# Kernel tuning notes

Hardware: AMD Instinct MI355X
Metric: run time of the kernel (lower is better)

The kernel has to match this reference:

```python
import jax, jax.numpy as jnp
import numpy as np
from math import comb

# --- module hyperparameters (from init_kwargs / module-level constants) ---
F = 32          # features
NITER = 3       # num_iterations
NB = 16         # num_basis_functions
NDCM = 4        # n_dcm
CUTOFF = 4.0
MAXZ = 17       # max_atomic_number
NC = 9          # (max_degree+1)^2 spherical components, max_degree=2
DEG = np.array([0, 1, 1, 1, 2, 2, 2, 2, 2])  # degree l of each component
BINOM = jnp.asarray([comb(NB - 1, k) for k in range(NB)], dtype=jnp.float32)


def _np_sph9(x, y, z):
    # real spherical harmonics up to l=2 on the unit sphere (numpy, for Gaunt table)
    c0 = 0.28209479177387814; c1 = 0.4886025119029199
    c2a = 1.0925484305920792; c2b = 0.31539156525252005; c2c = 0.5462742152960396
    return np.stack([c0 * np.ones_like(x), c1 * y, c1 * z, c1 * x,
                     c2a * x * y, c2a * y * z, c2b * (3.0 * z * z - 1.0),
                     c2a * x * z, c2c * (x * x - y * y)], axis=0)


def _gaunt():
    # real Gaunt (Clebsch-Gordan-type) coefficients G[a,b,c] = int Y_a Y_b Y_c dOmega
    # via Gauss-Legendre (cos theta) x midpoint (phi) quadrature -- exact for l<=2 products
    ct, wt = np.polynomial.legendre.leggauss(64)
    nph = 256
    phi = (np.arange(nph) + 0.5) * (2.0 * np.pi / nph)
    st = np.sqrt(1.0 - ct ** 2)
    x = st[:, None] * np.cos(phi)[None, :]
    y = st[:, None] * np.sin(phi)[None, :]
    z = np.broadcast_to(ct[:, None], x.shape)
    w = (wt[:, None] * (2.0 * np.pi / nph)) * np.ones((1, nph))
    Y = _np_sph9(x, y, z)
    G = np.einsum('aij,bij,cij,ij->abc', Y, Y, Y, w)
    G[np.abs(G) < 1e-6] = 0.0
    return G

CG = jnp.asarray(_gaunt(), dtype=jnp.float32)  # (9, 9, 9), sparse


def _sph9(u):
    # u: (E, 3) unit vectors -> (E, 9)
    x, y, z = u[:, 0], u[:, 1], u[:, 2]
    c0 = 0.28209479177387814; c1 = 0.4886025119029199
    c2a = 1.0925484305920792; c2b = 0.31539156525252005; c2c = 0.5462742152960396
    return jnp.stack([jnp.full_like(x, c0), c1 * y, c1 * z, c1 * x,
                      c2a * x * y, c2a * y * z, c2b * (3.0 * z * z - 1.0),
                      c2a * x * z, c2c * (x * x - y * y)], axis=-1)


def _radial(r):
    # reciprocal Bernstein radial basis * smooth cutoff; r: (E,) -> (E, NB)
    u = 1.0 / (1.0 + r)
    k = jnp.arange(NB, dtype=jnp.float32)
    rb = BINOM * u[:, None] ** k * (1.0 - u[:, None]) ** (NB - 1 - k)
    t = r / CUTOFF
    den = jnp.where(t < 1.0, 1.0 - t * t, 1.0)
    fc = jnp.where(t < 1.0, jnp.exp(-t * t / den), 0.0)  # smooth_cutoff
    return rb * fc[:, None]


def _equiv_dense(x, W, b=None):
    # per-degree linear (equivariant Dense): x (N, 9, Fin), W (3, Fin, Fout); bias on l=0 only
    y = jnp.einsum('ncf,cfg->ncg', x, W[DEG])
    if b is not None:
        y = y.at[:, 0, :].add(b)
    return y


def _tp(xs, bf):
    # Gaunt tensor-product contraction: out[e,c,f] = sum_ab CG[a,b,c] xs[e,a,f] bf[e,b,f]
    # loop over the 9 fixed output components to avoid an (E,9,9,F) intermediate
    out = []
    for c in range(NC):
        t = jnp.einsum('eaf,ab->ebf', xs, CG[:, :, c])
        out.append(jnp.sum(t * bf, axis=1))
    return jnp.stack(out, axis=1)


def _forward(atomic_numbers, positions, dst_idx, src_idx, embed, Wb, W1, b1, W2, b2,
             Wt00, Wt11, Wmono, element_bias):
    n = atomic_numbers.shape[0]
    disp = positions[src_idx] - positions[dst_idx]                 # (E, 3) gather
    r = jnp.sqrt(jnp.sum(disp * disp, axis=-1) + 1e-12)            # safe norm
    u = disp / r[:, None]
    basis = _sph9(u)[:, :, None] * _radial(r)[:, None, :]          # (E, 9, NB)
    x = jnp.zeros((n, NC, F), dtype=positions.dtype).at[:, 0, :].set(embed[atomic_numbers])
    for i in range(NITER):  # message passing iterations
        bf = jnp.einsum('ebn,bng->ebg', basis, Wb[i][DEG])         # per-degree radial->feature mix (E,9,F)
        msg = _tp(x[src_idx], bf)                                  # gather src + tensor product
        y = x + jax.ops.segment_sum(msg, dst_idx, num_segments=n)  # scatter-aggregate + residual add
        y = _equiv_dense(y, W1[i], b1[i])
        y = jax.nn.silu(y)
        y = _equiv_dense(y, W2[i], b2[i])
        x = x + y                                                  # residual update
    # TensorDense to n_dcm channels, then readout heads
    mono = (x[:, 0, :] @ Wt00) @ Wmono + element_bias[atomic_numbers][:, None]  # (N, NDCM)
    dip = jnp.einsum('ncf,fg->ncg', x[:, 1:4, :], Wt11)            # (N, 3, NDCM) vector channel
    dip = jnp.clip(jax.nn.silu(dip), -0.3, 0.3) + positions[:, :, None]
    return mono, dip


def setup_inputs():
    key = jax.random.key(0)
    ks = jax.random.split(key, 12)
    N, E = 10000, 160000
    return {
        'atomic_numbers': jax.random.randint(ks[0], (N,), 0, MAXZ + 1),
        'positions': jax.random.normal(ks[1], (N, 3), jnp.float32) * 3.0,
        'dst_idx': jax.random.randint(ks[2], (E,), 0, N),
        'src_idx': jax.random.randint(ks[3], (E,), 0, N),
        'embed': jax.random.normal(ks[4], (MAXZ + 1, F), jnp.float32),
        'Wb': jax.random.normal(ks[5], (NITER, 3, NB, F), jnp.float32) / np.sqrt(NB).astype(np.float32),
        'W1': jax.random.normal(ks[6], (NITER, 3, F, F), jnp.float32) / np.sqrt(F).astype(np.float32),
        'b1': jnp.zeros((NITER, F), jnp.float32),
        'W2': jax.random.normal(ks[7], (NITER, 3, F, F), jnp.float32) / np.sqrt(F).astype(np.float32),
        'b2': jnp.zeros((NITER, F), jnp.float32),
        'Wt00': jax.random.normal(ks[8], (F, NDCM), jnp.float32) / np.sqrt(F).astype(np.float32),
        'Wt11': jax.random.normal(ks[9], (F, NDCM), jnp.float32) / np.sqrt(F).astype(np.float32),
        'Wmono': jax.random.normal(ks[10], (NDCM, NDCM), jnp.float32) / np.sqrt(NDCM).astype(np.float32),
        'element_bias': jnp.zeros((MAXZ + 1,), jnp.float32),
    }


def reference(atomic_numbers, positions, dst_idx, src_idx, embed, Wb, W1, b1, W2, b2,
              Wt00, Wt11, Wmono, element_bias):
    return _forward(atomic_numbers, positions, dst_idx, src_idx, embed, Wb, W1, b1, W2, b2,
                    Wt00, Wt11, Wmono, element_bias)
```

## Files before the change

kernel.cpp:

```cpp
#include <hip/hip_runtime.h>
#include <hip/hip_bf16.h>


#define NITER 3
#define BCAP  64

#define OFF_WB    0
#define OFF_W1    4608
#define OFF_B1    13824
#define OFF_W2    13920
#define OFF_B2    23136
#define OFF_WT00  23232
#define OFF_WT11  23360
#define OFF_WMONO 23488
#define OFF_EB    23504
#define OFF_EMB   23522
#define WC_TOTAL  24098

__device__ __forceinline__ float b2f(const __hip_bfloat16 v) { return __bfloat162float(v); }

#define KC0 0.28209479177387814f
#define KG1 0.21850968611841584f
#define KG2 0.12615662610100802f
#define KG3 0.18022375157287861f
#define KG4 0.09011187578643931f
#define KG5 0.15607834722743988f

__device__ __forceinline__ float ldany(const void* p, int i, bool f32) {
    return f32 ? ((const float*)p)[i] : b2f(((const __hip_bfloat16*)p)[i]);
}

__device__ __forceinline__ bool wave_sniff(const void* pos) {
    const __hip_bfloat16* p = (const __hip_bfloat16*)pos;
    int lane = threadIdx.x & 63;
    int bad = 0;
    #pragma unroll
    for (int k = 0; k < 4; k++) {
        float v = b2f(p[lane + k*64]);
        bad |= !(fabsf(v) < 1.0e6f);
    }
    return __ballot(bad) != 0ull;
}

__global__ void setup_kernel(const void* pos, const void* Wb, const void* W1,
        const void* b1, const void* W2, const void* b2, const void* Wt00,
        const void* Wt11, const void* Wmono, const void* eb, const void* emb,
        const int* __restrict__ an,
        float* __restrict__ posf, float* __restrict__ wc,
        float* __restrict__ x, int N) {
    bool f32 = wave_sniff(pos);
    int i = blockIdx.x * blockDim.x + threadIdx.x;
    int np = N * 3;
    if (i < np) { posf[i] = ldany(pos, i, f32); return; }
    int j = i - np;
    if (j < WC_TOTAL) {
        const void* src; int rel;
        if      (j < OFF_W1)    { src = Wb;    rel = j; }
        else if (j < OFF_B1)    { src = W1;    rel = j - OFF_W1; }
        else if (j < OFF_W2)    { src = b1;    rel = j - OFF_B1; }
        else if (j < OFF_B2)    { src = W2;    rel = j - OFF_W2; }
        else if (j < OFF_WT00)  { src = b2;    rel = j - OFF_B2; }
        else if (j < OFF_WT11)  { src = Wt00;  rel = j - OFF_WT00; }
        else if (j < OFF_WMONO) { src = Wt11;  rel = j - OFF_WT11; }
        else if (j < OFF_EB)    { src = Wmono; rel = j - OFF_WMONO; }
        else if (j < OFF_EMB)   { src = eb;    rel = j - OFF_EB; }
        else                    { src = emb;   rel = j - OFF_EMB; }
        wc[j] = ldany(src, rel, f32);
        return;
    }
    j -= WC_TOTAL;
    if (j < N * 32) {
        int n = j >> 5, rem = j & 31;
        x[(size_t)n * 288 + rem] = ldany(emb, an[n] * 32 + rem, f32);
    }
}

__device__ __forceinline__ bool edge_geom(float dx, float dy, float dz,
                                          float* sp, float* rad) {
    float r2 = dx*dx + dy*dy + dz*dz + 1e-12f;
    if (r2 >= 16.0f) return false;
    float r  = sqrtf(r2);
    float t2 = r2 * 0.0625f;
    float fc = __expf(-t2 / (1.0f - t2));
    float u = 1.0f / (1.0f + r);
    float v = 1.0f - u;
    const float BIN[16] = {1.f,15.f,105.f,455.f,1365.f,3003.f,5005.f,6435.f,
                           6435.f,5005.f,3003.f,1365.f,455.f,105.f,15.f,1.f};
    float vp[16];
    vp[0] = 1.0f;
    #pragma unroll
    for (int k = 1; k < 16; k++) vp[k] = vp[k-1] * v;
    float up = 1.0f;
    #pragma unroll
    for (int n = 0; n < 16; n++) { rad[n] = BIN[n] * up * vp[15-n] * fc; up *= u; }
    float ir = 1.0f / r;
    float ux = dx*ir, uy = dy*ir, uz = dz*ir;
    const float c0 = 0.28209479177387814f, c1 = 0.4886025119029199f;
    const float c2a = 1.0925484305920792f, c2b = 0.31539156525252005f, c2c = 0.5462742152960396f;
    sp[0] = c0;
    sp[1] = c1*uy; sp[2] = c1*uz; sp[3] = c1*ux;
    sp[4] = c2a*ux*uy; sp[5] = c2a*uy*uz; sp[6] = c2b*(3.0f*uz*uz - 1.0f);
    sp[7] = c2a*ux*uz; sp[8] = c2c*(ux*ux - uy*uy);
    return true;
}

__global__ void fill_csr_kernel(const float* __restrict__ posf,
        const int* __restrict__ srcI, const int* __restrict__ dstI,
        float* __restrict__ geo2, int* __restrict__ cur, int E) {
    int e = blockIdx.x * blockDim.x + threadIdx.x;
    if (e >= E) return;
    int s = srcI[e], d = dstI[e];
    float sp[9], rad[16];
    if (!edge_geom(posf[s*3+0] - posf[d*3+0],
                   posf[s*3+1] - posf[d*3+1],
                   posf[s*3+2] - posf[d*3+2], sp, rad)) return;
    int slot = atomicAdd(&cur[d], 1);
    float* gp = geo2 + ((size_t)d * BCAP + slot) * 32;
    gp[0] = __int_as_float(s);
    gp[1] = 0.0f;
    #pragma unroll
    for (int a = 0; a < 9; a++) gp[2 + a] = sp[a];
    gp[11] = 0.0f;
    #pragma unroll
    for (int k = 0; k < 16; k++) gp[16 + k] = rad[k];
}

template <bool FIRST, bool LAST>
__global__ __launch_bounds__(256) void edge_gather_kernel(
        const float* __restrict__ x, float* __restrict__ y,
        const float* __restrict__ geo2, const int* __restrict__ cur,
        const float* __restrict__ Wbi, int N) {
    int f = threadIdx.x & 31;
    int n = (blockIdx.x * blockDim.x + threadIdx.x) >> 5;
    if (n >= N) return;
    float w0[16], w1[16], w2[16];
    #pragma unroll
    for (int k = 0; k < 16; k++) {
        w0[k] = Wbi[(0*16 + k)*32 + f];
        w1[k] = Wbi[(1*16 + k)*32 + f];
        w2[k] = Wbi[(2*16 + k)*32 + f];
    }
    float A0=0.f,A1=0.f,A2=0.f,A3=0.f,A4=0.f,A5=0.f,A6=0.f,A7=0.f,A8=0.f;
    int beg = n * BCAP, end = beg + cur[n];
    for (int e = beg; e < end; e++) {
        const float4* gp = (const float4*)(geo2 + (size_t)e * 32);
        float4 h0 = gp[0], h1 = gp[1], h2 = gp[2];
        float4 r0 = gp[4], r1 = gp[5], r2 = gp[6], r3 = gp[7];
        int s = __float_as_int(h0.x);
        float rad[16] = {r0.x,r0.y,r0.z,r0.w, r1.x,r1.y,r1.z,r1.w,
                         r2.x,r2.y,r2.z,r2.w, r3.x,r3.y,r3.z,r3.w};
        float rw0 = 0.f, rw1 = 0.f, rw2 = 0.f;
        #pragma unroll
        for (int k = 0; k < 16; k++) {
            rw0 = fmaf(rad[k], w0[k], rw0);
            rw1 = fmaf(rad[k], w1[k], rw1);
            rw2 = fmaf(rad[k], w2[k], rw2);
        }
        float B0 = h0.z*rw0;
        float B1 = h0.w*rw1, B2 = h1.x*rw1, B3 = h1.y*rw1;
        float B4 = h1.z*rw2, B5 = h1.w*rw2, B6 = h2.x*rw2,
              B7 = h2.y*rw2, B8 = h2.z*rw2;
        const float* xp = x + (size_t)s*288 + f;
        if (FIRST) {
            float X0 = xp[0];
            float k0 = KC0 * X0;
            A0 += k0*B0; A1 += k0*B1; A2 += k0*B2; A3 += k0*B3; A4 += k0*B4;
            A5 += k0*B5; A6 += k0*B6; A7 += k0*B7; A8 += k0*B8;
        } else {
            float X0 = xp[0],   X1 = xp[32],  X2 = xp[64],  X3 = xp[96],  X4 = xp[128];
            float X5 = xp[160], X6 = xp[192], X7 = xp[224], X8 = xp[256];
            A0 += KC0*(X0*B0 + X1*B1 + X2*B2 + X3*B3 + X4*B4 + X5*B5 + X6*B6 + X7*B7 + X8*B8);
            A1 += KC0*(X0*B1 + X1*B0) + KG1*(X3*B4 + X4*B3 + X2*B5 + X5*B2)
                - KG2*(X1*B6 + X6*B1) - KG1*(X1*B8 + X8*B1);
            A2 += KC0*(X0*B2 + X2*B0) + KG1*(X1*B5 + X5*B1 + X3*B7 + X7*B3)
                + 2.0f*KG2*(X2*B6 + X6*B2);
            A3 += KC0*(X0*B3 + X3*B0) + KG1*(X1*B4 + X4*B1 + X2*B7 + X7*B2)
                - KG2*(X3*B6 + X6*B3) + KG1*(X3*B8 + X8*B3);
            if (!LAST) {
                A4 += KC0*(X0*B4 + X4*B0) + KG1*(X1*B3 + X3*B1) + KG5*(X5*B7 + X7*B5)
                    - KG3*(X4*B6 + X6*B4);
                A5 += KC0*(X0*B5 + X5*B0) + KG1*(X1*B2 + X2*B1) + KG5*(X4*B7 + X7*B4)
                    + KG4*(X5*B6 + X6*B5) - KG5*(X5*B8 + X8*B5);
                A6 += KC0*(X0*B6 + X6*B0) - KG2*X1*B1 + 2.0f*KG2*X2*B2 - KG2*X3*B3
                    - KG3*X4*B4 + KG4*X5*B5 + KG3*X6*B6 + KG4*X7*B7 - KG3*X8*B8;
                A7 += KC0*(X0*B7 + X7*B0) + KG1*(X2*B3 + X3*B2) + KG5*(X4*B5 + X5*B4)
                    + KG4*(X6*B7 + X7*B6) + KG5*(X7*B8 + X8*B7);
                A8 += KC0*(X0*B8 + X8*B0) - KG1*X1*B1 + KG1*X3*B3 - KG5*X5*B5 + KG5*X7*B7
                    - KG3*(X6*B8 + X8*B6);
            }
        }
    }
    float* yp = y + (size_t)n * 288 + f;
    yp[0]   = A0; yp[32]  = A1; yp[64]  = A2; yp[96]  = A3;
    if (!LAST) {
        yp[128] = A4; yp[160] = A5; yp[192] = A6; yp[224] = A7; yp[256] = A8;
    }
}

template <bool FIRST>
__global__ __launch_bounds__(256) void atom_kernel(
        float* __restrict__ x, const float* __restrict__ y,
        const float* __restrict__ W1i, const float* __restrict__ b1i,
        const float* __restrict__ W2i, const float* __restrict__ b2i,
        int N) {
    __shared__ float sm[4][64*33];
    int lane  = threadIdx.x & 63;
    int wslot = threadIdx.x >> 6;
    int u = __builtin_amdgcn_readfirstlane(blockIdx.x * 4 + wslot);
    int t = u / 9;
    int c = u - t * 9;
    int d = (c == 0) ? 0 : ((c < 4) ? 1 : 2);
    const float* W1 = W1i + d * 1024;
    const float* W2 = W2i + d * 1024;
    float* tile = sm[wslot];
    bool usex = (!FIRST) || (c == 0);
    float4 xr4[8];
    #pragma unroll
    for (int k = 0; k < 8; k++) {
        int e  = lane * 4 + k * 256;
        int al = e >> 5, f = e & 31;
        int ag = t * 64 + al;
        float4 s = make_float4(0.f, 0.f, 0.f, 0.f);
        float4 xv = make_float4(0.f, 0.f, 0.f, 0.f);
        if (ag < N) {
            if (usex) xv = *(const float4*)(x + (size_t)ag * 288 + c * 32 + f);
            float4 yv = *(const float4*)(y + (size_t)ag * 288 + c * 32 + f);
            s = make_float4(xv.x + yv.x, xv.y + yv.y, xv.z + yv.z, xv.w + yv.w);
        }
        xr4[k] = xv;
        *(float4*)(tile + al * 33 + f) = s;
    }
    __syncthreads();
    float yin[32];
    #pragma unroll
    for (int k = 0; k < 8; k++) {
        float4 v = *(const float4*)(tile + lane * 33 + 4 * k);
        yin[4*k+0] = v.x; yin[4*k+1] = v.y; yin[4*k+2] = v.z; yin[4*k+3] = v.w;
    }
    float acc[32];
    #pragma unroll
    for (int g = 0; g < 32; g++) acc[g] = (c == 0) ? b1i[g] : 0.0f;
    #pragma unroll 4
    for (int fi = 0; fi < 32; fi++) {
        float v = yin[fi];
        #pragma unroll
        for (int g = 0; g < 32; g++) acc[g] = fmaf(v, W1[fi*32 + g], acc[g]);
    }
    #pragma unroll
    for (int g = 0; g < 32; g++)
        acc[g] = acc[g] * __builtin_amdgcn_rcpf(1.0f + __expf(-acc[g]));
    float out[32];
    #pragma unroll
    for (int g = 0; g < 32; g++) out[g] = (c == 0) ? b2i[g] : 0.0f;
    #pragma unroll 4
    for (int fi = 0; fi < 32; fi++) {
        float v = acc[fi];
        #pragma unroll
        for (int g = 0; g < 32; g++) out[g] = fmaf(v, W2[fi*32 + g], out[g]);
    }
    __syncthreads();
    #pragma unroll
    for (int k = 0; k < 8; k++)
        *(float4*)(tile + lane * 33 + 4 * k) =
            make_float4(out[4*k+0], out[4*k+1], out[4*k+2], out[4*k+3]);
    __syncthreads();
    #pragma unroll
    for (int k = 0; k < 8; k++) {
        int e  = lane * 4 + k * 256;
        int al = e >> 5, f = e & 31;
        int ag = t * 64 + al;
        if (ag < N) {
            float4 dv = *(const float4*)(tile + al * 33 + f);
            float4 xv = xr4[k];
            *(float4*)(x + (size_t)ag * 288 + c * 32 + f) =
                make_float4(xv.x + dv.x, xv.y + dv.y, xv.z + dv.z, xv.w + dv.w);
        }
    }
}

__global__ __launch_bounds__(256) void atom_readout_kernel(
        const float* __restrict__ x, const float* __restrict__ y,
        const float* __restrict__ W1i, const float* __restrict__ b1i,
        const float* __restrict__ W2i, const float* __restrict__ b2i,
        const int* __restrict__ an, const float* __restrict__ posf,
        const float* __restrict__ wc, const void* __restrict__ pos,
        void* __restrict__ out_, int N) {
    bool f32 = wave_sniff(pos);
    __shared__ float sm[4][64*33];
    int lane  = threadIdx.x & 63;
    int wslot = threadIdx.x >> 6;
    int c = __builtin_amdgcn_readfirstlane(wslot);
    int t = blockIdx.x;
    int d = (c == 0) ? 0 : 1;
    const float* W1 = W1i + d * 1024;
    const float* W2 = W2i + d * 1024;
    float* tile = sm[wslot];
    float4 xr4[8];
    #pragma unroll
    for (int k = 0; k < 8; k++) {
        int e  = lane * 4 + k * 256;
        int al = e >> 5, f = e & 31;
        int ag = t * 64 + al;
        float4 s = make_float4(0.f, 0.f, 0.f, 0.f);
        float4 xv = make_float4(0.f, 0.f, 0.f, 0.f);
        if (ag < N) {
            xv = *(const float4*)(x + (size_t)ag * 288 + c * 32 + f);
            float4 yv = *(const float4*)(y + (size_t)ag * 288 + c * 32 + f);
            s = make_float4(xv.x + yv.x, xv.y + yv.y, xv.z + yv.z, xv.w + yv.w);
        }
        xr4[k] = xv;
        *(float4*)(tile + al * 33 + f) = s;
    }
    __syncthreads();
    float yin[32];
    #pragma unroll
    for (int k = 0; k < 8; k++) {
        float4 v = *(const float4*)(tile + lane * 33 + 4 * k);
        yin[4*k+0] = v.x; yin[4*k+1] = v.y; yin[4*k+2] = v.z; yin[4*k+3] = v.w;
    }
    float acc[32];
    #pragma unroll
    for (int g = 0; g < 32; g++) acc[g] = (c == 0) ? b1i[g] : 0.0f;
    #pragma unroll 4
    for (int fi = 0; fi < 32; fi++) {
        float v = yin[fi];
        #pragma unroll
        for (int g = 0; g < 32; g++) acc[g] = fmaf(v, W1[fi*32 + g], acc[g]);
    }
    #pragma unroll
    for (int g = 0; g < 32; g++)
        acc[g] = acc[g] * __builtin_amdgcn_rcpf(1.0f + __expf(-acc[g]));
    float out[32];
    #pragma unroll
    for (int g = 0; g < 32; g++) out[g] = (c == 0) ? b2i[g] : 0.0f;
    #pragma unroll 4
    for (int fi = 0; fi < 32; fi++) {
        float v = acc[fi];
        #pragma unroll
        for (int g = 0; g < 32; g++) out[g] = fmaf(v, W2[fi*32 + g], out[g]);
    }
    __syncthreads();
    #pragma unroll
    for (int k = 0; k < 8; k++)
        *(float4*)(tile + lane * 33 + 4 * k) =
            make_float4(out[4*k+0], out[4*k+1], out[4*k+2], out[4*k+3]);
    __syncthreads();
    #pragma unroll
    for (int k = 0; k < 8; k++) {
        int e  = lane * 4 + k * 256;
        int al = e >> 5, f = e & 31;
        float4 dv = *(const float4*)(tile + al * 33 + f);
        float4 xv = xr4[k];
        *(float4*)(tile + al * 33 + f) =
            make_float4(xv.x + dv.x, xv.y + dv.y, xv.z + dv.z, xv.w + dv.w);
    }
    __syncthreads();
    if (threadIdx.x < 64) {
        int a  = threadIdx.x;
        int ag = t * 64 + a;
        if (ag < N) {
            const float* Wt00  = wc + OFF_WT00;
            const float* Wt11  = wc + OFF_WT11;
            const float* Wmono = wc + OFF_WMONO;
            const float* x0 = sm[0] + a * 33;
            float q[4] = {0.f, 0.f, 0.f, 0.f};
            for (int f = 0; f < 32; f++) {
                float xv = x0[f];
                #pragma unroll
                for (int j = 0; j < 4; j++) q[j] = fmaf(xv, Wt00[f*4 + j], q[j]);
            }
            float ebv = wc[OFF_EB + an[ag]];
            #pragma unroll
            for (int m = 0; m < 4; m++) {
                float accm = ebv;
                #pragma unroll
                for (int j = 0; j < 4; j++) accm = fmaf(q[j], Wmono[j*4 + m], accm);
                if (f32) ((float*)out_)[ag*4 + m] = accm;
                else ((__hip_bfloat16*)out_)[ag*4 + m] = __float2bfloat16(accm);
            }
            #pragma unroll
            for (int cc = 0; cc < 3; cc++) {
                float pc = posf[ag*3 + cc];
                const float* xc = sm[1 + cc] + a * 33;
                float dq[4] = {0.f, 0.f, 0.f, 0.f};
                for (int f = 0; f < 32; f++) {
                    float xv = xc[f];
                    #pragma unroll
                    for (int m = 0; m < 4; m++) dq[m] = fmaf(xv, Wt11[f*4 + m], dq[m]);
                }
                #pragma unroll
                for (int m = 0; m < 4; m++) {
                    float v = dq[m];
                    v = v * __builtin_amdgcn_rcpf(1.0f + __expf(-v));
                    v = fminf(fmaxf(v, -0.3f), 0.3f);
                    v += pc;
                    if (f32) ((float*)out_)[N*4 + ag*12 + cc*4 + m] = v;
                    else ((__hip_bfloat16*)out_)[N*4 + ag*12 + cc*4 + m] = __float2bfloat16(v);
                }
            }
        }
    }
}

__global__ void zero_kernel(float4* __restrict__ b, int n) {
    int i = blockIdx.x * blockDim.x + threadIdx.x;
    int stride = gridDim.x * blockDim.x;
    float4 z = make_float4(0.f, 0.f, 0.f, 0.f);
    for (; i < n; i += stride) b[i] = z;
}

__global__ __launch_bounds__(256) void edge_inline_kernel(
        const float* __restrict__ x, float* __restrict__ y,
        const float* __restrict__ posf,
        const int* __restrict__ srcI, const int* __restrict__ dstI,
        const float* __restrict__ Wbi, int E) {
    int f  = threadIdx.x & 31;
    int hw = (blockIdx.x * blockDim.x + threadIdx.x) >> 5;
    int nhw = gridDim.x * (blockDim.x >> 5);
    float w0[16], w1[16], w2[16];
    #pragma unroll
    for (int n = 0; n < 16; n++) {
        w0[n] = Wbi[(0*16 + n)*32 + f];
        w1[n] = Wbi[(1*16 + n)*32 + f];
        w2[n] = Wbi[(2*16 + n)*32 + f];
    }
    for (int e = hw; e < E; e += nhw) {
        int s = srcI[e], d = dstI[e];
        float sp[9], rad[16];
        if (!edge_geom(posf[s*3+0] - posf[d*3+0],
                       posf[s*3+1] - posf[d*3+1],
                       posf[s*3+2] - posf[d*3+2], sp, rad)) continue;
        float rw0 = 0.f, rw1 = 0.f, rw2 = 0.f;
        #pragma unroll
        for (int n = 0; n < 16; n++) {
            rw0 = fmaf(rad[n], w0[n], rw0);
            rw1 = fmaf(rad[n], w1[n], rw1);
            rw2 = fmaf(rad[n], w2[n], rw2);
        }
        float B0 = sp[0]*rw0;
        float B1 = sp[1]*rw1, B2 = sp[2]*rw1, B3 = sp[3]*rw1;
        float B4 = sp[4]*rw2, B5 = sp[5]*rw2, B6 = sp[6]*rw2,
              B7 = sp[7]*rw2, B8 = sp[8]*rw2;
        const float* xp = x + (size_t)s*288 + f;
        float X0 = xp[0],   X1 = xp[32],  X2 = xp[64],  X3 = xp[96],  X4 = xp[128];
        float X5 = xp[160], X6 = xp[192], X7 = xp[224], X8 = xp[256];
        float* yp = y + (size_t)d*288 + f;
        float m;
        m = KC0*(X0*B0 + X1*B1 + X2*B2 + X3*B3 + X4*B4 + X5*B5 + X6*B6 + X7*B7 + X8*B8);
        unsafeAtomicAdd(yp + 0, m);
        m = KC0*(X0*B1 + X1*B0) + KG1*(X3*B4 + X4*B3 + X2*B5 + X5*B2)
          - KG2*(X1*B6 + X6*B1) - KG1*(X1*B8 + X8*B1);
        unsafeAtomicAdd(yp + 32, m);
        m = KC0*(X0*B2 + X2*B0) + KG1*(X1*B5 + X5*B1 + X3*B7 + X7*B3)
          + 2.0f*KG2*(X2*B6 + X6*B2);
        unsafeAtomicAdd(yp + 64, m);
        m = KC0*(X0*B3 + X3*B0) + KG1*(X1*B4 + X4*B1 + X2*B7 + X7*B2)
          - KG2*(X3*B6 + X6*B3) + KG1*(X3*B8 + X8*B3);
        unsafeAtomicAdd(yp + 96, m);
        m = KC0*(X0*B4 + X4*B0) + KG1*(X1*B3 + X3*B1) + KG5*(X5*B7 + X7*B5)
          - KG3*(X4*B6 + X6*B4);
        unsafeAtomicAdd(yp + 128, m);
        m = KC0*(X0*B5 + X5*B0) + KG1*(X1*B2 + X2*B1) + KG5*(X4*B7 + X7*B4)
          + KG4*(X5*B6 + X6*B5) - KG5*(X5*B8 + X8*B5);
        unsafeAtomicAdd(yp + 160, m);
        m = KC0*(X0*B6 + X6*B0) - KG2*X1*B1 + 2.0f*KG2*X2*B2 - KG2*X3*B3
          - KG3*X4*B4 + KG4*X5*B5 + KG3*X6*B6 + KG4*X7*B7 - KG3*X8*B8;
        unsafeAtomicAdd(yp + 192, m);
        m = KC0*(X0*B7 + X7*B0) + KG1*(X2*B3 + X3*B2) + KG5*(X4*B5 + X5*B4)
          + KG4*(X6*B7 + X7*B6) + KG5*(X7*B8 + X8*B7);
        unsafeAtomicAdd(yp + 224, m);
        m = KC0*(X0*B8 + X8*B0) - KG1*X1*B1 + KG1*X3*B3 - KG5*X5*B5 + KG5*X7*B7
          - KG3*(X6*B8 + X8*B6);
        unsafeAtomicAdd(yp + 256, m);
    }
}

__global__ void readout_kernel(const float* __restrict__ x,
        const int* __restrict__ an, const float* __restrict__ posf,
        const float* __restrict__ wc, const void* __restrict__ pos,
        void* __restrict__ out, int N) {
    bool f32 = wave_sniff(pos);
    int n = blockIdx.x * blockDim.x + threadIdx.x;
    if (n >= N) return;
    const float* Wt00  = wc + OFF_WT00;
    const float* Wt11  = wc + OFF_WT11;
    const float* Wmono = wc + OFF_WMONO;
    const float* xb = x + (size_t)n * 288;
    float q[4] = {0.f, 0.f, 0.f, 0.f};
    for (int f = 0; f < 32; f++) {
        float xv = xb[f];
        #pragma unroll
        for (int j = 0; j < 4; j++) q[j] = fmaf(xv, Wt00[f*4 + j], q[j]);
    }
    float ebv = wc[OFF_EB + an[n]];
    #pragma unroll
    for (int m = 0; m < 4; m++) {
        float acc = ebv;
        #pragma unroll
        for (int j = 0; j < 4; j++) acc = fmaf(q[j], Wmono[j*4 + m], acc);
        if (f32) ((float*)out)[n*4 + m] = acc;
        else ((__hip_bfloat16*)out)[n*4 + m] = __float2bfloat16(acc);
    }
    #pragma unroll
    for (int c = 0; c < 3; c++) {
        float pc = posf[n*3 + c];
        const float* xc = xb + (1 + c)*32;
        float dq[4] = {0.f, 0.f, 0.f, 0.f};
        for (int f = 0; f < 32; f++) {
            float xv = xc[f];
            #pragma unroll
            for (int m = 0; m < 4; m++) dq[m] = fmaf(xv, Wt11[f*4 + m], dq[m]);
        }
        #pragma unroll
        for (int m = 0; m < 4; m++) {
            float v = dq[m];
            v = v * __builtin_amdgcn_rcpf(1.0f + __expf(-v));
            v = fminf(fmaxf(v, -0.3f), 0.3f);
            v += pc;
            if (f32) ((float*)out)[N*4 + n*12 + c*4 + m] = v;
            else ((__hip_bfloat16*)out)[N*4 + n*12 + c*4 + m] = __float2bfloat16(v);
        }
    }
}

extern "C" void kernel_launch(void* const* d_in, const int* in_sizes, int n_in,
                              void* d_out, int out_size, void* d_ws, size_t ws_size,
                              hipStream_t stream) {
    const int* an    = (const int*)d_in[0];
    const void* pos  = d_in[1];
    const int* dstI  = (const int*)d_in[2];
    const int* srcI  = (const int*)d_in[3];
    const void* embed= d_in[4];
    const void* Wb   = d_in[5];
    const void* W1   = d_in[6];
    const void* b1   = d_in[7];
    const void* W2   = d_in[8];
    const void* b2   = d_in[9];
    const void* Wt00 = d_in[10];
    const void* Wt11 = d_in[11];
    const void* Wmono= d_in[12];
    const void* eb   = d_in[13];
    int N = in_sizes[0];
    int E = in_sizes[2];

    float* x    = (float*)d_ws;
    float* y    = x + (size_t)N * 288;
    float* posf = y + (size_t)N * 288;
    float* wc   = posf + (size_t)N * 3;
    int* cur    = (int*)(wc + WC_TOTAL);
    uintptr_t ga = ((uintptr_t)(cur + N) + 127) & ~(uintptr_t)127;
    float* geo2 = (float*)ga;
    size_t need = (uintptr_t)(geo2 + (size_t)N * BCAP * 32) - (uintptr_t)d_ws;
    bool use_csr = (ws_size >= need);

    hipMemsetAsync(cur, 0, sizeof(int) * (size_t)N, stream);
    if (!use_csr)
        zero_kernel<<<512, 256, 0, stream>>>((float4*)x, N * 72);
    {
        int tot = N * 3 + WC_TOTAL + N * 32;
        setup_kernel<<<(tot + 255)/256, 256, 0, stream>>>(
            pos, Wb, W1, b1, W2, b2, Wt00, Wt11, Wmono, eb, embed,
            an, posf, wc, x, N);
    }
    int ntiles = (N + 63) / 64;
    if (use_csr) {
        fill_csr_kernel<<<(E + 255)/256, 256, 0, stream>>>(posf, srcI, dstI,
                                                           geo2, cur, E);
        int gblocks = (N + 7) / 8;
        for (int i = 0; i < NITER; i++) {
            const float* Wbi = wc + OFF_WB + (size_t)i*1536;
            const float* W1i = wc + OFF_W1 + (size_t)i*3072;
            const float* b1i = wc + OFF_B1 + (size_t)i*32;
            const float* W2i = wc + OFF_W2 + (size_t)i*3072;
            const float* b2i = wc + OFF_B2 + (size_t)i*32;
            if (i == 0) {
                edge_gather_kernel<true,false><<<gblocks, 256, 0, stream>>>(
                    x, y, geo2, cur, Wbi, N);
                atom_kernel<true><<<(ntiles*9 + 3)/4, 256, 0, stream>>>(
                    x, y, W1i, b1i, W2i, b2i, N);
            } else if (i == NITER - 1) {
                edge_gather_kernel<false,true><<<gblocks, 256, 0, stream>>>(
                    x, y, geo2, cur, Wbi, N);
                atom_readout_kernel<<<ntiles, 256, 0, stream>>>(
                    x, y, W1i, b1i, W2i, b2i, an, posf, wc, pos, d_out, N);
            } else {
                edge_gather_kernel<false,false><<<gblocks, 256, 0, stream>>>(
                    x, y, geo2, cur, Wbi, N);
                atom_kernel<false><<<(ntiles*9 + 3)/4, 256, 0, stream>>>(
                    x, y, W1i, b1i, W2i, b2i, N);
            }
        }
    } else {
        int ablocks = (ntiles * 9 + 3) / 4;
        for (int i = 0; i < NITER; i++) {
            zero_kernel<<<512, 256, 0, stream>>>((float4*)y, N * 72);
            edge_inline_kernel<<<2048, 256, 0, stream>>>(x, y, posf, srcI, dstI,
                wc + OFF_WB + (size_t)i*1536, E);
            atom_kernel<false><<<ablocks, 256, 0, stream>>>(x, y,
                wc + OFF_W1 + (size_t)i*3072, wc + OFF_B1 + (size_t)i*32,
                wc + OFF_W2 + (size_t)i*3072, wc + OFF_B2 + (size_t)i*32, N);
        }
        readout_kernel<<<(N + 255)/256, 256, 0, stream>>>(x, an, posf, wc, pos,
                                                          d_out, N);
    }
}
```

Before: 223.4 us.

## Fuse edge gather and atom MLP per iteration; fold CSR fill into setup

Each message-passing iteration now runs as one kernel per 32-atom tile: it gathers edge messages into shared memory and then applies the per-degree MLP update. Node features ping-pong between two buffers, which removes the intermediate y round-trip through global memory. Edge geometry and CSR bucket filling move into the setup kernel, dropping a separate launch. Both kernel launches and global traffic go down, but the fused kernel uses a larger shared-memory slab and has less parallelism per block.

```diff
diff --git a/kernel.cpp b/kernel.cpp
--- a/kernel.cpp
+++ b/kernel.cpp
@@ -42,12 +42,43 @@
     return __ballot(bad) != 0ull;
 }
 
+__device__ __forceinline__ bool edge_geom(float dx, float dy, float dz,
+                                          float* sp, float* rad) {
+    float r2 = dx*dx + dy*dy + dz*dz + 1e-12f;
+    if (r2 >= 16.0f) return false;
+    float r  = sqrtf(r2);
+    float t2 = r2 * 0.0625f;
+    float fc = __expf(-t2 / (1.0f - t2));
+    float u = 1.0f / (1.0f + r);
+    float v = 1.0f - u;
+    const float BIN[16] = {1.f,15.f,105.f,455.f,1365.f,3003.f,5005.f,6435.f,
+                           6435.f,5005.f,3003.f,1365.f,455.f,105.f,15.f,1.f};
+    float vp[16];
+    vp[0] = 1.0f;
+    #pragma unroll
+    for (int k = 1; k < 16; k++) vp[k] = vp[k-1] * v;
+    float up = 1.0f;
+    #pragma unroll
+    for (int n = 0; n < 16; n++) { rad[n] = BIN[n] * up * vp[15-n] * fc; up *= u; }
+    float ir = 1.0f / r;
+    float ux = dx*ir, uy = dy*ir, uz = dz*ir;
+    const float c0 = 0.28209479177387814f, c1 = 0.4886025119029199f;
+    const float c2a = 1.0925484305920792f, c2b = 0.31539156525252005f, c2c = 0.5462742152960396f;
+    sp[0] = c0;
+    sp[1] = c1*uy; sp[2] = c1*uz; sp[3] = c1*ux;
+    sp[4] = c2a*ux*uy; sp[5] = c2a*uy*uz; sp[6] = c2b*(3.0f*uz*uz - 1.0f);
+    sp[7] = c2a*ux*uz; sp[8] = c2c*(ux*ux - uy*uy);
+    return true;
+}
+
 __global__ void setup_kernel(const void* pos, const void* Wb, const void* W1,
         const void* b1, const void* W2, const void* b2, const void* Wt00,
         const void* Wt11, const void* Wmono, const void* eb, const void* emb,
         const int* __restrict__ an,
+        const int* __restrict__ srcI, const int* __restrict__ dstI,
         float* __restrict__ posf, float* __restrict__ wc,
-        float* __restrict__ x, int N) {
+        float* __restrict__ x, float* __restrict__ geo2, int* __restrict__ cur,
+        int N, int E, int use_csr) {
     bool f32 = wave_sniff(pos);
     int i = blockIdx.x * blockDim.x + threadIdx.x;
     int np = N * 3;
@@ -72,330 +103,246 @@
     if (j < N * 32) {
         int n = j >> 5, rem = j & 31;
         x[(size_t)n * 288 + rem] = ldany(emb, an[n] * 32 + rem, f32);
-    }
-}
-
-__device__ __forceinline__ bool edge_geom(float dx, float dy, float dz,
-                                          float* sp, float* rad) {
-    float r2 = dx*dx + dy*dy + dz*dz + 1e-12f;
-    if (r2 >= 16.0f) return false;
-    float r  = sqrtf(r2);
-    float t2 = r2 * 0.0625f;
-    float fc = __expf(-t2 / (1.0f - t2));
-    float u = 1.0f / (1.0f + r);
-    float v = 1.0f - u;
-    const float BIN[16] = {1.f,15.f,105.f,455.f,1365.f,3003.f,5005.f,6435.f,
-                           6435.f,5005.f,3003.f,1365.f,455.f,105.f,15.f,1.f};
-    float vp[16];
-    vp[0] = 1.0f;
-    #pragma unroll
-    for (int k = 1; k < 16; k++) vp[k] = vp[k-1] * v;
-    float up = 1.0f;
-    #pragma unroll
-    for (int n = 0; n < 16; n++) { rad[n] = BIN[n] * up * vp[15-n] * fc; up *= u; }
-    float ir = 1.0f / r;
-    float ux = dx*ir, uy = dy*ir, uz = dz*ir;
-    const float c0 = 0.28209479177387814f, c1 = 0.4886025119029199f;
-    const float c2a = 1.0925484305920792f, c2b = 0.31539156525252005f, c2c = 0.5462742152960396f;
-    sp[0] = c0;
-    sp[1] = c1*uy; sp[2] = c1*uz; sp[3] = c1*ux;
-    sp[4] = c2a*ux*uy; sp[5] = c2a*uy*uz; sp[6] = c2b*(3.0f*uz*uz - 1.0f);
-    sp[7] = c2a*ux*uz; sp[8] = c2c*(ux*ux - uy*uy);
-    return true;
-}
-
-__global__ void fill_csr_kernel(const float* __restrict__ posf,
-        const int* __restrict__ srcI, const int* __restrict__ dstI,
-        float* __restrict__ geo2, int* __restrict__ cur, int E) {
-    int e = blockIdx.x * blockDim.x + threadIdx.x;
-    if (e >= E) return;
-    int s = srcI[e], d = dstI[e];
-    float sp[9], rad[16];
-    if (!edge_geom(posf[s*3+0] - posf[d*3+0],
-                   posf[s*3+1] - posf[d*3+1],
-                   posf[s*3+2] - posf[d*3+2], sp, rad)) return;
-    int slot = atomicAdd(&cur[d], 1);
-    float* gp = geo2 + ((size_t)d * BCAP + slot) * 32;
-    gp[0] = __int_as_float(s);
-    gp[1] = 0.0f;
-    #pragma unroll
-    for (int a = 0; a < 9; a++) gp[2 + a] = sp[a];
-    gp[11] = 0.0f;
-    #pragma unroll
-    for (int k = 0; k < 16; k++) gp[16 + k] = rad[k];
+        return;
+    }
+    j -= N * 32;
+    if (j < E && use_csr) {
+        int s = srcI[j], d = dstI[j];
+        float sp[9], rad[16];
+        if (!edge_geom(ldany(pos, s*3+0, f32) - ldany(pos, d*3+0, f32),
+                       ldany(pos, s*3+1, f32) - ldany(pos, d*3+1, f32),
+                       ldany(pos, s*3+2, f32) - ldany(pos, d*3+2, f32),
+                       sp, rad)) return;
+        int slot = atomicAdd(&cur[d], 1);
+        float* gp = geo2 + ((size_t)d * BCAP + slot) * 32;
+        gp[0] = __int_as_float(s);
+        gp[1] = 0.0f;
+        #pragma unroll
+        for (int a = 0; a < 9; a++) gp[2 + a] = sp[a];
+        gp[11] = 0.0f;
+        #pragma unroll
+        for (int k = 0; k < 16; k++) gp[16 + k] = rad[k];
+    }
 }
 
 template <bool FIRST, bool LAST>
-__global__ __launch_bounds__(256) void edge_gather_kernel(
-        const float* __restrict__ x, float* __restrict__ y,
+__global__ __launch_bounds__(256) void fused_iter_kernel(
+        const float* __restrict__ xin, float* __restrict__ xout,
         const float* __restrict__ geo2, const int* __restrict__ cur,
-        const float* __restrict__ Wbi, int N) {
-    int f = threadIdx.x & 31;
-    int n = (blockIdx.x * blockDim.x + threadIdx.x) >> 5;
-    if (n >= N) return;
-    float w0[16], w1[16], w2[16];
-    #pragma unroll
-    for (int k = 0; k < 16; k++) {
-        w0[k] = Wbi[(0*16 + k)*32 + f];
-        w1[k] = Wbi[(1*16 + k)*32 + f];
-        w2[k] = Wbi[(2*16 + k)*32 + f];
-    }
-    float A0=0.f,A1=0.f,A2=0.f,A3=0.f,A4=0.f,A5=0.f,A6=0.f,A7=0.f,A8=0.f;
-    int beg = n * BCAP, end = beg + cur[n];
-    for (int e = beg; e < end; e++) {
-        const float4* gp = (const float4*)(geo2 + (size_t)e * 32);
-        float4 h0 = gp[0], h1 = gp[1], h2 = gp[2];
-        float4 r0 = gp[4], r1 = gp[5], r2 = gp[6], r3 = gp[7];
-        int s = __float_as_int(h0.x);
-        float rad[16] = {r0.x,r0.y,r0.z,r0.w, r1.x,r1.y,r1.z,r1.w,
-                         r2.x,r2.y,r2.z,r2.w, r3.x,r3.y,r3.z,r3.w};
-        float rw0 = 0.f, rw1 = 0.f, rw2 = 0.f;
-        #pragma unroll
-        for (int k = 0; k < 16; k++) {
-            rw0 = fmaf(rad[k], w0[k], rw0);
-            rw1 = fmaf(rad[k], w1[k], rw1);
-            rw2 = fmaf(rad[k], w2[k], rw2);
-        }
-        float B0 = h0.z*rw0;
-        float B1 = h0.w*rw1, B2 = h1.x*rw1, B3 = h1.y*rw1;
-        float B4 = h1.z*rw2, B5 = h1.w*rw2, B6 = h2.x*rw2,
-              B7 = h2.y*rw2, B8 = h2.z*rw2;
-        const float* xp = x + (size_t)s*288 + f;
-        if (FIRST) {
-            float X0 = xp[0];
-            float k0 = KC0 * X0;
-            A0 += k0*B0; A1 += k0*B1; A2 += k0*B2; A3 += k0*B3; A4 += k0*B4;
-            A5 += k0*B5; A6 += k0*B6; A7 += k0*B7; A8 += k0*B8;
-        } else {
-            float X0 = xp[0],   X1 = xp[32],  X2 = xp[64],  X3 = xp[96],  X4 = xp[128];
-            float X5 = xp[160], X6 = xp[192], X7 = xp[224], X8 = xp[256];
-            A0 += KC0*(X0*B0 + X1*B1 + X2*B2 + X3*B3 + X4*B4 + X5*B5 + X6*B6 + X7*B7 + X8*B8);
-            A1 += KC0*(X0*B1 + X1*B0) + KG1*(X3*B4 + X4*B3 + X2*B5 + X5*B2)
-                - KG2*(X1*B6 + X6*B1) - KG1*(X1*B8 + X8*B1);
-            A2 += KC0*(X0*B2 + X2*B0) + KG1*(X1*B5 + X5*B1 + X3*B7 + X7*B3)
-                + 2.0f*KG2*(X2*B6 + X6*B2);
-            A3 += KC0*(X0*B3 + X3*B0) + KG1*(X1*B4 + X4*B1 + X2*B7 + X7*B2)
-                - KG2*(X3*B6 + X6*B3) + KG1*(X3*B8 + X8*B3);
-            if (!LAST) {
-                A4 += KC0*(X0*B4 + X4*B0) + KG1*(X1*B3 + X3*B1) + KG5*(X5*B7 + X7*B5)
-                    - KG3*(X4*B6 + X6*B4);
-                A5 += KC0*(X0*B5 + X5*B0) + KG1*(X1*B2 + X2*B1) + KG5*(X4*B7 + X7*B4)
-                    + KG4*(X5*B6 + X6*B5) - KG5*(X5*B8 + X8*B5);
-                A6 += KC0*(X0*B6 + X6*B0) - KG2*X1*B1 + 2.0f*KG2*X2*B2 - KG2*X3*B3
-                    - KG3*X4*B4 + KG4*X5*B5 + KG3*X6*B6 + KG4*X7*B7 - KG3*X8*B8;
-                A7 += KC0*(X0*B7 + X7*B0) + KG1*(X2*B3 + X3*B2) + KG5*(X4*B5 + X5*B4)
-                    + KG4*(X6*B7 + X7*B6) + KG5*(X7*B8 + X8*B7);
-                A8 += KC0*(X0*B8 + X8*B0) - KG1*X1*B1 + KG1*X3*B3 - KG5*X5*B5 + KG5*X7*B7
-                    - KG3*(X6*B8 + X8*B6);
-            }
-        }
-    }
-    float* yp = y + (size_t)n * 288 + f;
-    yp[0]   = A0; yp[32]  = A1; yp[64]  = A2; yp[96]  = A3;
-    if (!LAST) {
-        yp[128] = A4; yp[160] = A5; yp[192] = A6; yp[224] = A7; yp[256] = A8;
-    }
-}
-
-template <bool FIRST>
-__global__ __launch_bounds__(256) void atom_kernel(
-        float* __restrict__ x, const float* __restrict__ y,
-        const float* __restrict__ W1i, const float* __restrict__ b1i,
-        const float* __restrict__ W2i, const float* __restrict__ b2i,
-        int N) {
-    __shared__ float sm[4][64*33];
-    int lane  = threadIdx.x & 63;
-    int wslot = threadIdx.x >> 6;
-    int u = __builtin_amdgcn_readfirstlane(blockIdx.x * 4 + wslot);
-    int t = u / 9;
-    int c = u - t * 9;
-    int d = (c == 0) ? 0 : ((c < 4) ? 1 : 2);
-    const float* W1 = W1i + d * 1024;
-    const float* W2 = W2i + d * 1024;
-    float* tile = sm[wslot];
-    bool usex = (!FIRST) || (c == 0);
-    float4 xr4[8];
-    #pragma unroll
-    for (int k = 0; k < 8; k++) {
-        int e  = lane * 4 + k * 256;
-        int al = e >> 5, f = e & 31;
-        int ag = t * 64 + al;
-        float4 s = make_float4(0.f, 0.f, 0.f, 0.f);
-        float4 xv = make_float4(0.f, 0.f, 0.f, 0.f);
-        if (ag < N) {
-            if (usex) xv = *(const float4*)(x + (size_t)ag * 288 + c * 32 + f);
-            float4 yv = *(const float4*)(y + (size_t)ag * 288 + c * 32 + f);
-            s = make_float4(xv.x + yv.x, xv.y + yv.y, xv.z + yv.z, xv.w + yv.w);
-        }
-        xr4[k] = xv;
-        *(float4*)(tile + al * 33 + f) = s;
-    }
-    __syncthreads();
-    float yin[32];
-    #pragma unroll
-    for (int k = 0; k < 8; k++) {
-        float4 v = *(const float4*)(tile + lane * 33 + 4 * k);
-        yin[4*k+0] = v.x; yin[4*k+1] = v.y; yin[4*k+2] = v.z; yin[4*k+3] = v.w;
-    }
-    float acc[32];
-    #pragma unroll
-    for (int g = 0; g < 32; g++) acc[g] = (c == 0) ? b1i[g] : 0.0f;
-    #pragma unroll 4
-    for (int fi = 0; fi < 32; fi++) {
-        float v = yin[fi];
-        #pragma unroll
-        for (int g = 0; g < 32; g++) acc[g] = fmaf(v, W1[fi*32 + g], acc[g]);
-    }
-    #pragma unroll
-    for (int g = 0; g < 32; g++)
-        acc[g] = acc[g] * __builtin_amdgcn_rcpf(1.0f + __expf(-acc[g]));
-    float out[32];
-    #pragma unroll
-    for (int g = 0; g < 32; g++) out[g] = (c == 0) ? b2i[g] : 0.0f;
-    #pragma unroll 4
-    for (int fi = 0; fi < 32; fi++) {
-        float v = acc[fi];
-        #pragma unroll
-        for (int g = 0; g < 32; g++) out[g] = fmaf(v, W2[fi*32 + g], out[g]);
-    }
-    __syncthreads();
-    #pragma unroll
-    for (int k = 0; k < 8; k++)
-        *(float4*)(tile + lane * 33 + 4 * k) =
-            make_float4(out[4*k+0], out[4*k+1], out[4*k+2], out[4*k+3]);
-    __syncthreads();
-    #pragma unroll
-    for (int k = 0; k < 8; k++) {
-        int e  = lane * 4 + k * 256;
-        int al = e >> 5, f = e & 31;
-        int ag = t * 64 + al;
-        if (ag < N) {
-            float4 dv = *(const float4*)(tile + al * 33 + f);
-            float4 xv = xr4[k];
-            *(float4*)(x + (size_t)ag * 288 + c * 32 + f) =
-                make_float4(xv.x + dv.x, xv.y + dv.y, xv.z + dv.z, xv.w + dv.w);
-        }
-    }
-}
-
-__global__ __launch_bounds__(256) void atom_readout_kernel(
-        const float* __restrict__ x, const float* __restrict__ y,
+        const float* __restrict__ Wbi,
         const float* __restrict__ W1i, const float* __restrict__ b1i,
         const float* __restrict__ W2i, const float* __restrict__ b2i,
         const int* __restrict__ an, const float* __restrict__ posf,
         const float* __restrict__ wc, const void* __restrict__ pos,
         void* __restrict__ out_, int N) {
-    bool f32 = wave_sniff(pos);
-    __shared__ float sm[4][64*33];
-    int lane  = threadIdx.x & 63;
-    int wslot = threadIdx.x >> 6;
-    int c = __builtin_amdgcn_readfirstlane(wslot);
-    int t = blockIdx.x;
-    int d = (c == 0) ? 0 : 1;
-    const float* W1 = W1i + d * 1024;
-    const float* W2 = W2i + d * 1024;
-    float* tile = sm[wslot];
-    float4 xr4[8];
-    #pragma unroll
-    for (int k = 0; k < 8; k++) {
-        int e  = lane * 4 + k * 256;
-        int al = e >> 5, f = e & 31;
-        int ag = t * 64 + al;
-        float4 s = make_float4(0.f, 0.f, 0.f, 0.f);
-        float4 xv = make_float4(0.f, 0.f, 0.f, 0.f);
-        if (ag < N) {
-            xv = *(const float4*)(x + (size_t)ag * 288 + c * 32 + f);
-            float4 yv = *(const float4*)(y + (size_t)ag * 288 + c * 32 + f);
-            s = make_float4(xv.x + yv.x, xv.y + yv.y, xv.z + yv.z, xv.w + yv.w);
-        }
-        xr4[k] = xv;
-        *(float4*)(tile + al * 33 + f) = s;
+    constexpr int NCH_ = LAST ? 4 : 9;
+    __shared__ float slab[NCH_][32*33];
+    int tid = threadIdx.x;
+    int f   = tid & 31;
+    int hw  = tid >> 5;
+    int t   = blockIdx.x;
+    {
+        float w0[16], w1[16], w2[16];
+        #pragma unroll
+        for (int k = 0; k < 16; k++) {
+            w0[k] = Wbi[(0*16 + k)*32 + f];
+            w1[k] = Wbi[(1*16 + k)*32 + f];
+            w2[k] = Wbi[(2*16 + k)*32 + f];
+        }
+        for (int a4 = 0; a4 < 4; a4++) {
+            int al = hw * 4 + a4;
+            int n  = t * 32 + al;
+            float A0=0.f,A1=0.f,A2=0.f,A3=0.f,A4=0.f,A5=0.f,A6=0.f,A7=0.f,A8=0.f;
+            if (n < N) {
+                int beg = n * BCAP, end = beg + cur[n];
+                for (int e = beg; e < end; e++) {
+                    const float4* gp = (const float4*)(geo2 + (size_t)e * 32);
+                    float4 h0 = gp[0], h1 = gp[1], h2 = gp[2];
+                    float4 r0 = gp[4], r1 = gp[5], r2 = gp[6], r3 = gp[7];
+                    int s = __float_as_int(h0.x);
+                    float rad[16] = {r0.x,r0.y,r0.z,r0.w, r1.x,r1.y,r1.z,r1.w,
+                                     r2.x,r2.y,r2.z,r2.w, r3.x,r3.y,r3.z,r3.w};
+                    float rw0 = 0.f, rw1 = 0.f, rw2 = 0.f;
+                    #pragma unroll
+                    for (int k = 0; k < 16; k++) {
+                        rw0 = fmaf(rad[k], w0[k], rw0);
+                        rw1 = fmaf(rad[k], w1[k], rw1);
+                        rw2 = fmaf(rad[k], w2[k], rw2);
+                    }
+                    float B0 = h0.z*rw0;
+                    float B1 = h0.w*rw1, B2 = h1.x*rw1, B3 = h1.y*rw1;
+                    float B4 = h1.z*rw2, B5 = h1.w*rw2, B6 = h2.x*rw2,
+                          B7 = h2.y*rw2, B8 = h2.z*rw2;
+                    const float* xp = xin + (size_t)s*288 + f;
+                    if (FIRST) {
+                        float k0 = KC0 * xp[0];
+                        A0 += k0*B0; A1 += k0*B1; A2 += k0*B2; A3 += k0*B3;
+                        A4 += k0*B4; A5 += k0*B5; A6 += k0*B6; A7 += k0*B7;
+                        A8 += k0*B8;
+                    } else {
+                        float X0 = xp[0],   X1 = xp[32],  X2 = xp[64],  X3 = xp[96],  X4 = xp[128];
+                        float X5 = xp[160], X6 = xp[192], X7 = xp[224], X8 = xp[256];
+                        A0 += KC0*(X0*B0 + X1*B1 + X2*B2 + X3*B3 + X4*B4 + X5*B5 + X6*B6 + X7*B7 + X8*B8);
+                        A1 += KC0*(X0*B1 + X1*B0) + KG1*(X3*B4 + X4*B3 + X2*B5 + X5*B2)
+                            - KG2*(X1*B6 + X6*B1) - KG1*(X1*B8 + X8*B1);
+                        A2 += KC0*(X0*B2 + X2*B0) + KG1*(X1*B5 + X5*B1 + X3*B7 + X7*B3)
+                            + 2.0f*KG2*(X2*B6 + X6*B2);
+                        A3 += KC0*(X0*B3 + X3*B0) + KG1*(X1*B4 + X4*B1 + X2*B7 + X7*B2)
+                            - KG2*(X3*B6 + X6*B3) + KG1*(X3*B8 + X8*B3);
+                        if (!LAST) {
+                            A4 += KC0*(X0*B4 + X4*B0) + KG1*(X1*B3 + X3*B1) + KG5*(X5*B7 + X7*B5)
+                                - KG3*(X4*B6 + X6*B4);
+                            A5 += KC0*(X0*B5 + X5*B0) + KG1*(X1*B2 + X2*B1) + KG5*(X4*B7 + X7*B4)
+                                + KG4*(X5*B6 + X6*B5) - KG5*(X5*B8 + X8*B5);
+                            A6 += KC0*(X0*B6 + X6*B0) - KG2*X1*B1 + 2.0f*KG2*X2*B2 - KG2*X3*B3
+                                - KG3*X4*B4 + KG4*X5*B5 + KG3*X6*B6 + KG4*X7*B7 - KG3*X8*B8;
+                            A7 += KC0*(X0*B7 + X7*B0) + KG1*(X2*B3 + X3*B2) + KG5*(X4*B5 + X5*B4)
+                                + KG4*(X6*B7 + X7*B6) + KG5*(X7*B8 + X8*B7);
+                            A8 += KC0*(X0*B8 + X8*B0) - KG1*X1*B1 + KG1*X3*B3 - KG5*X5*B5 + KG5*X7*B7
+                                - KG3*(X6*B8 + X8*B6);
+                        }
+                    }
+                }
+                const float* xp = xin + (size_t)n*288 + f;
+                A0 += xp[0];
+                if (!FIRST) {
+                    A1 += xp[32]; A2 += xp[64]; A3 += xp[96];
+                    if (!LAST) {
+                        A4 += xp[128]; A5 += xp[160]; A6 += xp[192];
+                        A7 += xp[224]; A8 += xp[256];
+                    }
+                }
+                if (!FIRST && LAST) {  }
+            }
+            slab[0][al*33 + f] = A0;
+            slab[1][al*33 + f] = A1;
+            slab[2][al*33 + f] = A2;
+            slab[3][al*33 + f] = A3;
+            if (!LAST) {
+                slab[4][al*33 + f] = A4;
+                slab[5][al*33 + f] = A5;
+                slab[6][al*33 + f] = A6;
+                slab[7][al*33 + f] = A7;
+                slab[8][al*33 + f] = A8;
+            }
+        }
     }
     __syncthreads();
-    float yin[32];
-    #pragma unroll
-    for (int k = 0; k < 8; k++) {
-        float4 v = *(const float4*)(tile + lane * 33 + 4 * k);
-        yin[4*k+0] = v.x; yin[4*k+1] = v.y; yin[4*k+2] = v.z; yin[4*k+3] = v.w;
-    }
-    float acc[32];
-    #pragma unroll
-    for (int g = 0; g < 32; g++) acc[g] = (c == 0) ? b1i[g] : 0.0f;
-    #pragma unroll 4
-    for (int fi = 0; fi < 32; fi++) {
-        float v = yin[fi];
-        #pragma unroll
-        for (int g = 0; g < 32; g++) acc[g] = fmaf(v, W1[fi*32 + g], acc[g]);
-    }
-    #pragma unroll
-    for (int g = 0; g < 32; g++)
-        acc[g] = acc[g] * __builtin_amdgcn_rcpf(1.0f + __expf(-acc[g]));
-    float out[32];
-    #pragma unroll
-    for (int g = 0; g < 32; g++) out[g] = (c == 0) ? b2i[g] : 0.0f;
-    #pragma unroll 4
-    for (int fi = 0; fi < 32; fi++) {
-        float v = acc[fi];
-        #pragma unroll
-        for (int g = 0; g < 32; g++) out[g] = fmaf(v, W2[fi*32 + g], out[g]);
+    {
+        int wv   = tid >> 6;
+        int lane = tid & 63;
+        for (int c = wv; c < NCH_; c += 4) {
+            int d = (c == 0) ? 0 : ((c < 4) ? 1 : 2);
+            const float* W1 = W1i + d * 1024;
+            const float* W2 = W2i + d * 1024;
+            if (lane < 32) {
+                int al = lane;
+                float yin[32];
+                #pragma unroll
+                for (int k = 0; k < 8; k++) {
+                    float4 v = *(const float4*)(&slab[c][al*33 + 4*k]);
+                    yin[4*k+0] = v.x; yin[4*k+1] = v.y;
+                    yin[4*k+2] = v.z; yin[4*k+3] = v.w;
+                }
+                float acc[32];
+                #pragma unroll
+                for (int g = 0; g < 32; g++) acc[g] = (c == 0) ? b1i[g] : 0.0f;
+                #pragma unroll 4
+                for (int fi = 0; fi < 32; fi++) {
+                    float v = yin[fi];
+                    #pragma unroll
+                    for (int g = 0; g < 32; g++) acc[g] = fmaf(v, W1[fi*32 + g], acc[g]);
+                }
+                #pragma unroll
+                for (int g = 0; g < 32; g++)
+                    acc[g] = acc[g] * __builtin_amdgcn_rcpf(1.0f + __expf(-acc[g]));
+                float out[32];
+                #pragma unroll
+                for (int g = 0; g < 32; g++) out[g] = (c == 0) ? b2i[g] : 0.0f;
+                #pragma unroll 4
+                for (int fi = 0; fi < 32; fi++) {
+                    float v = acc[fi];
+                    #pragma unroll
+                    for (int g = 0; g < 32; g++) out[g] = fmaf(v, W2[fi*32 + g], out[g]);
+                }
+                #pragma unroll
+                for (int k = 0; k < 8; k++)
+                    *(float4*)(&slab[c][al*33 + 4*k]) =
+                        make_float4(out[4*k+0], out[4*k+1], out[4*k+2], out[4*k+3]);
+            }
+        }
     }
     __syncthreads();
-    #pragma unroll
-    for (int k = 0; k < 8; k++)
-        *(float4*)(tile + lane * 33 + 4 * k) =
-            make_float4(out[4*k+0], out[4*k+1], out[4*k+2], out[4*k+3]);
-    __syncthreads();
-    #pragma unroll
-    for (int k = 0; k < 8; k++) {
-        int e  = lane * 4 + k * 256;
-        int al = e >> 5, f = e & 31;
-        float4 dv = *(const float4*)(tile + al * 33 + f);
-        float4 xv = xr4[k];
-        *(float4*)(tile + al * 33 + f) =
-            make_float4(xv.x + dv.x, xv.y + dv.y, xv.z + dv.z, xv.w + dv.w);
-    }
-    __syncthreads();
-    if (threadIdx.x < 64) {
-        int a  = threadIdx.x;
-        int ag = t * 64 + a;
-        if (ag < N) {
-            const float* Wt00  = wc + OFF_WT00;
-            const float* Wt11  = wc + OFF_WT11;
-            const float* Wmono = wc + OFF_WMONO;
-            const float* x0 = sm[0] + a * 33;
-            float q[4] = {0.f, 0.f, 0.f, 0.f};
-            for (int f = 0; f < 32; f++) {
-                float xv = x0[f];
-                #pragma unroll
-                for (int j = 0; j < 4; j++) q[j] = fmaf(xv, Wt00[f*4 + j], q[j]);
+    if (!LAST) {
+        for (int idx = tid; idx < 32 * NCH_ * 8; idx += 256) {
+            int al = idx / (NCH_*8), rem = idx % (NCH_*8);
+            int c = rem >> 3, k = rem & 7;
+            int ag = t * 32 + al;
+            if (ag < N) {
+                const float* sp = &slab[0][0] + c*(32*33) + al*33 + 4*k;
+                float4 dv = make_float4(sp[0], sp[1], sp[2], sp[3]);
+                float4 xv = make_float4(0.f, 0.f, 0.f, 0.f);
+                if (!FIRST || c == 0)
+                    xv = *(const float4*)(xin + (size_t)ag*288 + c*32 + 4*k);
+                *(float4*)(xout + (size_t)ag*288 + c*32 + 4*k) =
+                    make_float4(xv.x + dv.x, xv.y + dv.y, xv.z + dv.z, xv.w + dv.w);
             }
-            float ebv = wc[OFF_EB + an[ag]];
-            #pragma unroll
-            for (int m = 0; m < 4; m++) {
-                float accm = ebv;
-                #pragma unroll
-                for (int j = 0; j < 4; j++) accm = fmaf(q[j], Wmono[j*4 + m], accm);
-                if (f32) ((float*)out_)[ag*4 + m] = accm;
-                else ((__hip_bfloat16*)out_)[ag*4 + m] = __float2bfloat16(accm);
+        }
+    } else {
+        bool f32 = wave_sniff(pos);
+        for (int idx = tid; idx < 32 * 4 * 8; idx += 256) {
+            int al = idx >> 5, rem = idx & 31;
+            int c = rem >> 3, k = rem & 7;
+            int ag = t * 32 + al;
+            if (ag < N) {
+                float* sp = &slab[0][0] + c*(32*33) + al*33 + 4*k;
+                const float* xp = xin + (size_t)ag*288 + c*32 + 4*k;
+                sp[0] += xp[0]; sp[1] += xp[1]; sp[2] += xp[2]; sp[3] += xp[3];
             }
-            #pragma unroll
-            for (int cc = 0; cc < 3; cc++) {
-                float pc = posf[ag*3 + cc];
-                const float* xc = sm[1 + cc] + a * 33;
-                float dq[4] = {0.f, 0.f, 0.f, 0.f};
-                for (int f = 0; f < 32; f++) {
-                    float xv = xc[f];
+        }
+        __syncthreads();
+        if (tid < 32) {
+            int a  = tid;
+            int ag = t * 32 + a;
+            if (ag < N) {
+                const float* Wt00  = wc + OFF_WT00;
+                const float* Wt11  = wc + OFF_WT11;
+                const float* Wmono = wc + OFF_WMONO;
+                const float* x0 = &slab[0][0] + a * 33;
+                float q[4] = {0.f, 0.f, 0.f, 0.f};
+                for (int ff = 0; ff < 32; ff++) {
+                    float xv = x0[ff];
                     #pragma unroll
-                    for (int m = 0; m < 4; m++) dq[m] = fmaf(xv, Wt11[f*4 + m], dq[m]);
-                }
+                    for (int j = 0; j < 4; j++) q[j] = fmaf(xv, Wt00[ff*4 + j], q[j]);
+                }
+                float ebv = wc[OFF_EB + an[ag]];
                 #pragma unroll
                 for (int m = 0; m < 4; m++) {
-                    float v = dq[m];
-                    v = v * __builtin_amdgcn_rcpf(1.0f + __expf(-v));
-                    v = fminf(fmaxf(v, -0.3f), 0.3f);
-                    v += pc;
-                    if (f32) ((float*)out_)[N*4 + ag*12 + cc*4 + m] = v;
-                    else ((__hip_bfloat16*)out_)[N*4 + ag*12 + cc*4 + m] = __float2bfloat16(v);
+                    float accm = ebv;
+                    #pragma unroll
+                    for (int j = 0; j < 4; j++) accm = fmaf(q[j], Wmono[j*4 + m], accm);
+                    if (f32) ((float*)out_)[ag*4 + m] = accm;
+                    else ((__hip_bfloat16*)out_)[ag*4 + m] = __float2bfloat16(accm);
+                }
+                #pragma unroll
+                for (int cc = 0; cc < 3; cc++) {
+                    float pc = posf[ag*3 + cc];
+                    const float* xc = &slab[0][0] + (1 + cc)*(32*33) + a * 33;
+                    float dq[4] = {0.f, 0.f, 0.f, 0.f};
+                    for (int ff = 0; ff < 32; ff++) {
+                        float xv = xc[ff];
+                        #pragma unroll
+                        for (int m = 0; m < 4; m++) dq[m] = fmaf(xv, Wt11[ff*4 + m], dq[m]);
+                    }
+                    #pragma unroll
+                    for (int m = 0; m < 4; m++) {
+                        float v = dq[m];
+                        v = v * __builtin_amdgcn_rcpf(1.0f + __expf(-v));
+                        v = fminf(fmaxf(v, -0.3f), 0.3f);
+                        v += pc;
+                        if (f32) ((float*)out_)[N*4 + ag*12 + cc*4 + m] = v;
+                        else ((__hip_bfloat16*)out_)[N*4 + ag*12 + cc*4 + m] = __float2bfloat16(v);
+                    }
                 }
             }
         }
@@ -475,6 +422,85 @@
     }
 }
 
+__global__ __launch_bounds__(256) void atom_kernel(
+        float* __restrict__ x, const float* __restrict__ y,
+        const float* __restrict__ W1i, const float* __restrict__ b1i,
+        const float* __restrict__ W2i, const float* __restrict__ b2i,
+        int N) {
+    __shared__ float sm[4][64*33];
+    int lane  = threadIdx.x & 63;
+    int wslot = threadIdx.x >> 6;
+    int u = __builtin_amdgcn_readfirstlane(blockIdx.x * 4 + wslot);
+    int t = u / 9;
+    int c = u - t * 9;
+    int d = (c == 0) ? 0 : ((c < 4) ? 1 : 2);
+    const float* W1 = W1i + d * 1024;
+    const float* W2 = W2i + d * 1024;
+    float* tile = sm[wslot];
+    float4 xr4[8];
+    #pragma unroll
+    for (int k = 0; k < 8; k++) {
+        int e  = lane * 4 + k * 256;
+        int al = e >> 5, f = e & 31;
+        int ag = t * 64 + al;
+        float4 s = make_float4(0.f, 0.f, 0.f, 0.f);
+        float4 xv = make_float4(0.f, 0.f, 0.f, 0.f);
+        if (ag < N) {
+            xv = *(const float4*)(x + (size_t)ag * 288 + c * 32 + f);
+            float4 yv = *(const float4*)(y + (size_t)ag * 288 + c * 32 + f);
+            s = make_float4(xv.x + yv.x, xv.y + yv.y, xv.z + yv.z, xv.w + yv.w);
+        }
+        xr4[k] = xv;
+        *(float4*)(tile + al * 33 + f) = s;
+    }
+    __syncthreads();
+    float yin[32];
+    #pragma unroll
+    for (int k = 0; k < 8; k++) {
+        float4 v = *(const float4*)(tile + lane * 33 + 4 * k);
+        yin[4*k+0] = v.x; yin[4*k+1] = v.y; yin[4*k+2] = v.z; yin[4*k+3] = v.w;
+    }
+    float acc[32];
+    #pragma unroll
+    for (int g = 0; g < 32; g++) acc[g] = (c == 0) ? b1i[g] : 0.0f;
+    #pragma unroll 4
+    for (int fi = 0; fi < 32; fi++) {
+        float v = yin[fi];
+        #pragma unroll
+        for (int g = 0; g < 32; g++) acc[g] = fmaf(v, W1[fi*32 + g], acc[g]);
+    }
+    #pragma unroll
+    for (int g = 0; g < 32; g++)
+        acc[g] = acc[g] * __builtin_amdgcn_rcpf(1.0f + __expf(-acc[g]));
+    float out[32];
+    #pragma unroll
+    for (int g = 0; g < 32; g++) out[g] = (c == 0) ? b2i[g] : 0.0f;
+    #pragma unroll 4
+    for (int fi = 0; fi < 32; fi++) {
+        float v = acc[fi];
+        #pragma unroll
+        for (int g = 0; g < 32; g++) out[g] = fmaf(v, W2[fi*32 + g], out[g]);
+    }
+    __syncthreads();
+    #pragma unroll
+    for (int k = 0; k < 8; k++)
+        *(float4*)(tile + lane * 33 + 4 * k) =
+            make_float4(out[4*k+0], out[4*k+1], out[4*k+2], out[4*k+3]);
+    __syncthreads();
+    #pragma unroll
+    for (int k = 0; k < 8; k++) {
+        int e  = lane * 4 + k * 256;
+        int al = e >> 5, f = e & 31;
+        int ag = t * 64 + al;
+        if (ag < N) {
+            float4 dv = *(const float4*)(tile + al * 33 + f);
+            float4 xv = xr4[k];
+            *(float4*)(x + (size_t)ag * 288 + c * 32 + f) =
+                make_float4(xv.x + dv.x, xv.y + dv.y, xv.z + dv.z, xv.w + dv.w);
+        }
+    }
+}
+
 __global__ void readout_kernel(const float* __restrict__ x,
         const int* __restrict__ an, const float* __restrict__ posf,
         const float* __restrict__ wc, const void* __restrict__ pos,
@@ -543,9 +569,9 @@
     int N = in_sizes[0];
     int E = in_sizes[2];
 
-    float* x    = (float*)d_ws;
-    float* y    = x + (size_t)N * 288;
-    float* posf = y + (size_t)N * 288;
+    float* xA   = (float*)d_ws;
+    float* xB   = xA + (size_t)N * 288;
+    float* posf = xB + (size_t)N * 288;
     float* wc   = posf + (size_t)N * 3;
     int* cur    = (int*)(wc + WC_TOTAL);
     uintptr_t ga = ((uintptr_t)(cur + N) + 127) & ~(uintptr_t)127;
@@ -555,48 +581,39 @@
 
     hipMemsetAsync(cur, 0, sizeof(int) * (size_t)N, stream);
     if (!use_csr)
-        zero_kernel<<<512, 256, 0, stream>>>((float4*)x, N * 72);
+        zero_kernel<<<512, 256, 0, stream>>>((float4*)xA, N * 72);
     {
-        int tot = N * 3 + WC_TOTAL + N * 32;
+        int tot = N * 3 + WC_TOTAL + N * 32 + (use_csr ? E : 0);
         setup_kernel<<<(tot + 255)/256, 256, 0, stream>>>(
             pos, Wb, W1, b1, W2, b2, Wt00, Wt11, Wmono, eb, embed,
-            an, posf, wc, x, N);
-    }
-    int ntiles = (N + 63) / 64;
+            an, srcI, dstI, posf, wc, xA, geo2, cur, N, E, use_csr ? 1 : 0);
+    }
     if (use_csr) {
-        fill_csr_kernel<<<(E + 255)/256, 256, 0, stream>>>(posf, srcI, dstI,
-                                                           geo2, cur, E);
-        int gblocks = (N + 7) / 8;
-        for (int i = 0; i < NITER; i++) {
-            const float* Wbi = wc + OFF_WB + (size_t)i*1536;
-            const float* W1i = wc + OFF_W1 + (size_t)i*3072;
-            const float* b1i = wc + OFF_B1 + (size_t)i*32;
-            const float* W2i = wc + OFF_W2 + (size_t)i*3072;
-            const float* b2i = wc + OFF_B2 + (size_t)i*32;
-            if (i == 0) {
-                edge_gather_kernel<true,false><<<gblocks, 256, 0, stream>>>(
-                    x, y, geo2, cur, Wbi, N);
-                atom_kernel<true><<<(ntiles*9 + 3)/4, 256, 0, stream>>>(
-                    x, y, W1i, b1i, W2i, b2i, N);
-            } else if (i == NITER - 1) {
-                edge_gather_kernel<false,true><<<gblocks, 256, 0, stream>>>(
-                    x, y, geo2, cur, Wbi, N);
-                atom_readout_kernel<<<ntiles, 256, 0, stream>>>(
-                    x, y, W1i, b1i, W2i, b2i, an, posf, wc, pos, d_out, N);
-            } else {
-                edge_gather_kernel<false,false><<<gblocks, 256, 0, stream>>>(
-                    x, y, geo2, cur, Wbi, N);
-                atom_kernel<false><<<(ntiles*9 + 3)/4, 256, 0, stream>>>(
-                    x, y, W1i, b1i, W2i, b2i, N);
-            }
-        }
+        int tiles32 = (N + 31) / 32;
+        fused_iter_kernel<true,false><<<tiles32, 256, 0, stream>>>(
+            xA, xB, geo2, cur,
+            wc + OFF_WB, wc + OFF_W1, wc + OFF_B1, wc + OFF_W2, wc + OFF_B2,
+            an, posf, wc, pos, d_out, N);
+        fused_iter_kernel<false,false><<<tiles32, 256, 0, stream>>>(
+            xB, xA, geo2, cur,
+            wc + OFF_WB + 1536, wc + OFF_W1 + 3072, wc + OFF_B1 + 32,
+            wc + OFF_W2 + 3072, wc + OFF_B2 + 32,
+            an, posf, wc, pos, d_out, N);
+        fused_iter_kernel<false,true><<<tiles32, 256, 0, stream>>>(
+            xA, nullptr, geo2, cur,
+            wc + OFF_WB + 3072, wc + OFF_W1 + 6144, wc + OFF_B1 + 64,
+            wc + OFF_W2 + 6144, wc + OFF_B2 + 64,
+            an, posf, wc, pos, d_out, N);
     } else {
+        float* x = xA;
+        float* y = xB;
+        int ntiles = (N + 63) / 64;
         int ablocks = (ntiles * 9 + 3) / 4;
         for (int i = 0; i < NITER; i++) {
             zero_kernel<<<512, 256, 0, stream>>>((float4*)y, N * 72);
             edge_inline_kernel<<<2048, 256, 0, stream>>>(x, y, posf, srcI, dstI,
                 wc + OFF_WB + (size_t)i*1536, E);
-            atom_kernel<false><<<ablocks, 256, 0, stream>>>(x, y,
+            atom_kernel<<<ablocks, 256, 0, stream>>>(x, y,
                 wc + OFF_W1 + (size_t)i*3072, wc + OFF_B1 + (size_t)i*32,
                 wc + OFF_W2 + (size_t)i*3072, wc + OFF_B2 + (size_t)i*32, N);
         }
```

Measured after the change: 353.6 us. 58.3% more time.
